# Kernel tuning notes

Hardware: AMD Instinct MI355X
Metric: run time of the kernel (lower is better)

## Reference

```python
import jax, jax.numpy as jnp
import numpy as np

LN_EPS = 1e-12


def _layernorm(x, gamma, beta):
    mu = jnp.mean(x, axis=-1, keepdims=True)
    var = jnp.var(x, axis=-1, keepdims=True)
    return gamma * (x - mu) / jnp.sqrt(var + LN_EPS) + beta


def setup_inputs() -> dict:
    key = jax.random.key(0)
    ks = jax.random.split(key, 8)
    B, N, C, H = 8, 8192, 512, 8
    FFN = 4 * C
    s_attn = 1.0 / np.sqrt(C)
    s_ffn1 = 1.0 / np.sqrt(C)
    s_ffn2 = 1.0 / np.sqrt(FFN)
    return {
        "x": jax.random.normal(ks[0], (B, N, C), jnp.float32),
        "wq": jax.random.normal(ks[1], (C, C), jnp.float32) * s_attn,
        "bq": jnp.zeros((C,), jnp.float32),
        "wk": jax.random.normal(ks[2], (C, C), jnp.float32) * s_attn,
        "bk": jnp.zeros((C,), jnp.float32),
        "wv": jax.random.normal(ks[3], (C, C), jnp.float32) * s_attn,
        "bv": jnp.zeros((C,), jnp.float32),
        "wo": jax.random.normal(ks[4], (C, C), jnp.float32) * s_attn,
        "bo": jnp.zeros((C,), jnp.float32),
        "gamma1": jnp.ones((C,), jnp.float32),
        "beta1": jnp.zeros((C,), jnp.float32),
        "w_fc1": jax.random.normal(ks[5], (C, FFN), jnp.float32) * s_ffn1,
        "b_fc1": jnp.zeros((FFN,), jnp.float32),
        "w_fc2": jax.random.normal(ks[6], (FFN, C), jnp.float32) * s_ffn2,
        "b_fc2": jnp.zeros((C,), jnp.float32),
        "gamma2": jnp.ones((C,), jnp.float32),
        "beta2": jnp.zeros((C,), jnp.float32),
        "window_size": 64,
        "n_head": 8,
    }


def reference(x, wq, bq, wk, bk, wv, bv, wo, bo, gamma1, beta1,
              w_fc1, b_fc1, w_fc2, b_fc2, gamma2, beta2,
              window_size, n_head):
    B, N, C = x.shape
    ws = window_size
    H = n_head
    dh = C // H

    # window partition: [B, N, C] -> [B*N/ws, ws, C]
    xw = x.reshape(B * N // ws, ws, C)
    shortcut = xw

    # windowed multi-head self-attention
    q = (xw @ wq + bq).reshape(-1, ws, H, dh)
    k = (xw @ wk + bk).reshape(-1, ws, H, dh)
    v = (xw @ wv + bv).reshape(-1, ws, H, dh)
    scale = 1.0 / jnp.sqrt(jnp.asarray(dh, xw.dtype))
    attn = jnp.einsum('wqhd,wkhd->whqk', q, k) * scale  # [nw, H, ws, ws]
    attn = jax.nn.softmax(attn, axis=-1)
    out = jnp.einsum('whqk,wkhd->wqhd', attn, v).reshape(-1, ws, C)
    out = out @ wo + bo

    # residual + LN1
    h = _layernorm(out + shortcut, gamma1, beta1)

    # MLP (fc1 -> GELU -> fc2), residual + LN2
    ff = jax.nn.gelu(h @ w_fc1 + b_fc1, approximate=False) @ w_fc2 + b_fc2
    h = _layernorm(ff + h, gamma2, beta2)

    # window reverse: -> [B, N, C]
    return h.reshape(B, N, C)
```

## Files before the change

kernel.cpp:

```cpp
#include <hip/hip_runtime.h>

typedef __attribute__((ext_vector_type(8))) short bf16x8;
typedef __attribute__((ext_vector_type(4))) float f32x4;

__device__ __forceinline__ short f2b(float f) {
  unsigned u = __builtin_bit_cast(unsigned, f);
  unsigned r = (u + 0x7FFFu + ((u >> 16) & 1u)) >> 16;
  return (short)r;
}
__device__ __forceinline__ float b2f(short s) {
  unsigned u = ((unsigned)(unsigned short)s) << 16;
  return __builtin_bit_cast(float, u);
}

__device__ __forceinline__ void gload16(const void* g, void* l) {
  __builtin_amdgcn_global_load_lds(
      (const __attribute__((address_space(1))) void*)g,
      (__attribute__((address_space(3))) void*)l, 16, 0, 0);
}

__device__ __forceinline__ float gelu_f(float v) {
  float u = v * (0.7978845608f + 0.0356774081f * v * v);
  float a = fabsf(u);
  float e = __expf(-2.f * a);
  float t = (1.f - e) * __builtin_amdgcn_rcpf(1.f + e);
  t = (u < 0.f) ? -t : t;
  return 0.5f * v * (1.f + t);
}

__global__ void cvt_bf16_vec(const float* __restrict__ src, short* __restrict__ dst, long n) {
  long i = ((long)blockIdx.x * 256 + threadIdx.x) * 8;
  if (i >= n) return;
  f32x4 a = *(const f32x4*)(src + i);
  f32x4 b = *(const f32x4*)(src + i + 4);
  bf16x8 o;
#pragma unroll
  for (int j = 0; j < 4; j++) o[j] = f2b(a[j]);
#pragma unroll
  for (int j = 0; j < 4; j++) o[j + 4] = f2b(b[j]);
  *(bf16x8*)(dst + i) = o;
}

__global__ void transpose_cvt_t(const float* __restrict__ src, short* __restrict__ dst,
                                int K, int N) {
  __shared__ float tile[32][33];
  const int n0 = blockIdx.x * 32, k0 = blockIdx.y * 32;
  const int j = threadIdx.x & 31, i0 = threadIdx.x >> 5;
#pragma unroll
  for (int r = 0; r < 4; r++) {
    int i = i0 + r * 8;
    tile[i][j] = src[(long)(k0 + i) * N + n0 + j];
  }
  __syncthreads();
#pragma unroll
  for (int r = 0; r < 4; r++) {
    int i = i0 + r * 8;
    dst[(long)(n0 + i) * K + k0 + j] = f2b(tile[j][i]);
  }
}

__global__ void pack_bias3(const float* __restrict__ b0, const float* __restrict__ b1,
                           const float* __restrict__ b2, float* __restrict__ out) {
  int t = blockIdx.x * 256 + threadIdx.x;
  if (t >= 1536) return;
  out[t] = (t < 512) ? b0[t] : ((t < 1024) ? b1[t - 512] : b2[t - 1024]);
}

template <int EPI>
__global__ __launch_bounds__(256, 3) void gemm_bt(
    const short* __restrict__ A, const short* __restrict__ Bt,
    const float* __restrict__ bias, const float* __restrict__ resF,
    const short* __restrict__ resB, void* __restrict__ Cout, int K, int ldc, int gxN) {
  __shared__ short lds[3 * 8192];
  const int t = threadIdx.x;
  const int w = t >> 6, lane = t & 63;
  const int lr = lane & 15, lg = lane >> 4;

  const int nwg = gridDim.x;
  const int orig = blockIdx.x;
  const int q = nwg >> 3, r = nwg & 7, xcd = orig & 7, idx = orig >> 3;
  const int swz = (xcd < r ? xcd * (q + 1) : r * (q + 1) + (xcd - r) * q) + idx;
  const long m0 = (long)(swz / gxN) * 128;
  const int n0 = (swz % gxN) * 128;

  const int wm = (w >> 1) * 64, wn = (w & 1) * 64;

  f32x4 acc[4][4];
#pragma unroll
  for (int i = 0; i < 4; i++)
#pragma unroll
    for (int j = 0; j < 4; j++) acc[i][j] = f32x4{0.f, 0.f, 0.f, 0.f};

  const int srow = t >> 2;
  const int schunk = (t & 3) ^ ((t >> 3) & 3);
  const short* Ag = A + (m0 + srow) * (long)K + schunk * 8;
  const short* Bg = Bt + ((long)n0 + srow) * K + schunk * 8;
  const long half = (long)64 * K;

#define STAGE(b, kt)                                   \
  {                                                    \
    short* d = lds + (b) * 8192 + t * 8;               \
    gload16(Ag + (long)(kt) * 32, d);                  \
    gload16(Ag + half + (long)(kt) * 32, d + 2048);    \
    gload16(Bg + (long)(kt) * 32, d + 4096);           \
    gload16(Bg + half + (long)(kt) * 32, d + 6144);    \
  }

  const int xsw = (lg ^ ((lr >> 1) & 3)) * 8;
  const int aoff = (wm + lr) * 32 + xsw;
  const int boff = 4096 + (wn + lr) * 32 + xsw;

#define TILE_WAIT(WN)                                        \
  asm volatile("s_waitcnt vmcnt(" #WN ")" ::: "memory");     \
  __builtin_amdgcn_sched_barrier(0);                         \
  __builtin_amdgcn_s_barrier();                              \
  __builtin_amdgcn_sched_barrier(0);

#define BODY(CB)                                                               \
  {                                                                            \
    const short* Lb = lds + (CB) * 8192;                                       \
    bf16x8 a[4], b[4];                                                         \
    _Pragma("unroll") for (int mi = 0; mi < 4; mi++)                           \
        a[mi] = *(const bf16x8*)(Lb + aoff + mi * 512);                        \
    _Pragma("unroll") for (int nj = 0; nj < 4; nj++)                           \
        b[nj] = *(const bf16x8*)(Lb + boff + nj * 512);                        \
    __builtin_amdgcn_s_setprio(1);                                             \
    _Pragma("unroll") for (int mi = 0; mi < 4; mi++)                           \
        _Pragma("unroll") for (int nj = 0; nj < 4; nj++) acc[mi][nj] =         \
            __builtin_amdgcn_mfma_f32_16x16x32_bf16(a[mi], b[nj], acc[mi][nj], \
                                                    0, 0, 0);                  \
    __builtin_amdgcn_s_setprio(0);                                             \
  }

  const int NKT = K >> 5;
  STAGE(0, 0)
  STAGE(1, 1)

  int cb = 0, sb = 2;
  for (int kt = 0; kt < NKT - 1; ++kt) {
    TILE_WAIT(4)
    if (kt + 2 < NKT) STAGE(sb, kt + 2)
    BODY(cb)
    cb = (cb == 2) ? 0 : cb + 1;
    sb = (sb == 2) ? 0 : sb + 1;
  }
  TILE_WAIT(0)
  BODY(cb)
#undef STAGE
#undef TILE_WAIT
#undef BODY

  float bv[4];
#pragma unroll
  for (int nj = 0; nj < 4; nj++) bv[nj] = bias[n0 + wn + nj * 16 + lr];

#pragma unroll
  for (int mi = 0; mi < 4; mi++)
#pragma unroll
    for (int i = 0; i < 4; i++) {
      const long row = m0 + wm + mi * 16 + lg * 4 + i;
      const long rb = row * ldc + n0 + wn + lr;
      if (EPI == 0) {
        short* p = (short*)Cout + rb;
#pragma unroll
        for (int nj = 0; nj < 4; nj++) p[nj * 16] = f2b(acc[mi][nj][i] + bv[nj]);
      } else if (EPI == 1) {
        short* p = (short*)Cout + rb;
#pragma unroll
        for (int nj = 0; nj < 4; nj++) p[nj * 16] = f2b(gelu_f(acc[mi][nj][i] + bv[nj]));
      } else if (EPI == 2) {
        short* p = (short*)Cout + rb;
        const float* rp = resF + rb;
#pragma unroll
        for (int nj = 0; nj < 4; nj++) p[nj * 16] = f2b(acc[mi][nj][i] + bv[nj] + rp[nj * 16]);
      } else {
        float* p = (float*)Cout + rb;
        const short* rp = resB + rb;
#pragma unroll
        for (int nj = 0; nj < 4; nj++)
          p[nj * 16] = acc[mi][nj][i] + bv[nj] + b2f(rp[nj * 16]);
      }
    }
}

#define DSR(d, a, OFF) \
  asm volatile("ds_read_b128 %0, %1 offset:" OFF : "=v"(d) : "v"(a))
#define SB __builtin_amdgcn_sched_barrier(0)

template <int EPI>
__global__ __launch_bounds__(512, 1) void gemm256(
    const short* __restrict__ A, const short* __restrict__ Bt,
    const float* __restrict__ bias, const float* __restrict__ resF,
    const short* __restrict__ resB, void* __restrict__ Cout, int K, int ldc, int gxN) {
  extern __shared__ short lds[];
  const int t = threadIdx.x;
  const int lane = t & 63, w = t >> 6;
  const int lr = lane & 15, lg = lane >> 4;
  const int wm = w >> 2, wn = w & 3;

  const int nwg = gridDim.x, orig = blockIdx.x;
  const int q8 = nwg >> 3, r8 = nwg & 7, xcd = orig & 7, idx = orig >> 3;
  const int swz = (xcd < r8 ? xcd * (q8 + 1) : r8 * (q8 + 1) + (xcd - r8) * q8) + idx;
  const long m0 = (long)(swz / gxN) * 256;
  const int n0 = (swz % gxN) * 256;

  f32x4 acc[8][4];
#pragma unroll
  for (int i = 0; i < 8; i++)
#pragma unroll
    for (int j = 0; j < 4; j++) acc[i][j] = f32x4{0.f, 0.f, 0.f, 0.f};

  const int srow = t >> 3;
  const int sch = (t & 7) ^ (srow & 7);
  const short* sA = A + (m0 + srow) * (long)K + sch * 8;
  const short* sB = Bt + ((long)n0 + srow) * K + sch * 8;
  const long r64 = (long)64 * K;

#define STG_A(tt, h)                                                     \
  {                                                                      \
    short* d_ = lds + ((tt) & 1) * 16384 + (h) * 8192 + t * 8;           \
    const short* s_ = sA + (h) * 2 * r64 + (long)(tt) * 64;              \
    gload16(s_, d_);                                                     \
    gload16(s_ + r64, d_ + 4096);                                        \
  }
#define STG_B(tt, h)                                                     \
  {                                                                      \
    short* d_ = lds + 32768 + ((tt) & 1) * 16384 + (h) * 8192 + t * 8;   \
    const short* s_ = sB + (h) * 2 * r64 + (long)(tt) * 64;              \
    gload16(s_, d_);                                                     \
    gload16(s_ + r64, d_ + 4096);                                        \
  }

  const unsigned ldsB = (unsigned)(uintptr_t)lds;
  const unsigned xb0 = (unsigned)((lg ^ (lr & 7)) * 16);
  const unsigned xb1 = (unsigned)(((4 + lg) ^ (lr & 7)) * 16);
  const unsigned aRowB = (unsigned)((wm * 128 + lr) * 128);
  const unsigned bRowB = 65536u + (unsigned)((wn * 64 + lr) * 128);

#define BAR                                  \
  {                                          \
    SB;                                      \
    __builtin_amdgcn_s_barrier();            \
    SB;                                      \
  }
#define LGKM0 asm volatile("s_waitcnt lgkmcnt(0)")

  const int NT = K >> 6;
  STG_A(0, 0) STG_A(0, 1) STG_B(0, 0) STG_B(0, 1) STG_B(1, 0) STG_B(1, 1)
  asm volatile("s_waitcnt vmcnt(4)" ::: "memory");
  BAR

#define MFMA8(AC, A0, A1)                                                      \
  {                                                                            \
    __builtin_amdgcn_s_setprio(1);                                             \
    acc[AC][0] = __builtin_amdgcn_mfma_f32_16x16x32_bf16(A0, b00, acc[AC][0], 0, 0, 0); \
    acc[AC][0] = __builtin_amdgcn_mfma_f32_16x16x32_bf16(A1, b01, acc[AC][0], 0, 0, 0); \
    acc[AC][1] = __builtin_amdgcn_mfma_f32_16x16x32_bf16(A0, b10, acc[AC][1], 0, 0, 0); \
    acc[AC][1] = __builtin_amdgcn_mfma_f32_16x16x32_bf16(A1, b11, acc[AC][1], 0, 0, 0); \
    acc[AC][2] = __builtin_amdgcn_mfma_f32_16x16x32_bf16(A0, b20, acc[AC][2], 0, 0, 0); \
    acc[AC][2] = __builtin_amdgcn_mfma_f32_16x16x32_bf16(A1, b21, acc[AC][2], 0, 0, 0); \
    acc[AC][3] = __builtin_amdgcn_mfma_f32_16x16x32_bf16(A0, b30, acc[AC][3], 0, 0, 0); \
    acc[AC][3] = __builtin_amdgcn_mfma_f32_16x16x32_bf16(A1, b31, acc[AC][3], 0, 0, 0); \
    __builtin_amdgcn_s_setprio(0);                                             \
  }

  for (int tt = 0; tt < NT; ++tt) {
    const unsigned dAb = (unsigned)((tt & 1) * 32768);
    const unsigned aA0 = ldsB + aRowB + xb0 + dAb;
    const unsigned aA1 = ldsB + aRowB + xb1 + dAb;
    const unsigned bA0 = ldsB + bRowB + xb0 + dAb;
    const unsigned bA1 = ldsB + bRowB + xb1 + dAb;
    bf16x8 b00, b01, b10, b11, b20, b21, b30, b31;

    {
      DSR(b00, bA0, "0");    DSR(b01, bA1, "0");
      DSR(b10, bA0, "2048"); DSR(b11, bA1, "2048");
      DSR(b20, bA0, "4096"); DSR(b21, bA1, "4096");
      DSR(b30, bA0, "6144"); DSR(b31, bA1, "6144");
      bf16x8 a00, a01, a10, a11;
      DSR(a00, aA0, "0");    DSR(a01, aA1, "0");
      DSR(a10, aA0, "2048"); DSR(a11, aA1, "2048");
      SB;
      if (tt + 1 < NT) STG_A(tt + 1, 0)
      BAR
      LGKM0; SB;
      MFMA8(0, a00, a01)
      MFMA8(1, a10, a11)
      BAR
    }
    {
      bf16x8 a00, a01, a10, a11;
      DSR(a00, aA0, "4096"); DSR(a01, aA1, "4096");
      DSR(a10, aA0, "6144"); DSR(a11, aA1, "6144");
      SB;
      if (tt + 1 < NT) STG_A(tt + 1, 1)
      BAR
      LGKM0; SB;
      MFMA8(2, a00, a01)
      MFMA8(3, a10, a11)
      BAR
    }
    {
      bf16x8 a00, a01, a10, a11;
      DSR(a00, aA0, "8192");  DSR(a01, aA1, "8192");
      DSR(a10, aA0, "10240"); DSR(a11, aA1, "10240");
      SB;
      if (tt + 2 < NT) STG_B(tt + 2, 0)
      BAR
      LGKM0; SB;
      MFMA8(4, a00, a01)
      MFMA8(5, a10, a11)
      BAR
    }
    {
      bf16x8 a00, a01, a10, a11;
      DSR(a00, aA0, "12288"); DSR(a01, aA1, "12288");
      DSR(a10, aA0, "14336"); DSR(a11, aA1, "14336");
      SB;
      if (tt + 2 < NT) STG_B(tt + 2, 1)
      BAR
      LGKM0; SB;
      MFMA8(6, a00, a01)
      MFMA8(7, a10, a11)
      if (tt + 2 < NT) {
        asm volatile("s_waitcnt vmcnt(4)" ::: "memory");
      } else if (tt + 1 < NT) {
        asm volatile("s_waitcnt vmcnt(0)" ::: "memory");
      }
      BAR
    }
  }
#undef MFMA8
#undef STG_A
#undef STG_B

  float bv[4];
#pragma unroll
  for (int nj = 0; nj < 4; nj++) bv[nj] = bias[n0 + wn * 64 + nj * 16 + lr];

#pragma unroll
  for (int a = 0; a < 8; a++)
#pragma unroll
    for (int i = 0; i < 4; i++) {
      const long row = m0 + wm * 128 + a * 16 + lg * 4 + i;
      const long rb = row * ldc + n0 + wn * 64 + lr;
      if (EPI == 0) {
        short* p = (short*)Cout + rb;
#pragma unroll
        for (int nj = 0; nj < 4; nj++) p[nj * 16] = f2b(acc[a][nj][i] + bv[nj]);
      } else if (EPI == 1) {
        short* p = (short*)Cout + rb;
#pragma unroll
        for (int nj = 0; nj < 4; nj++) p[nj * 16] = f2b(gelu_f(acc[a][nj][i] + bv[nj]));
      } else if (EPI == 2) {
        short* p = (short*)Cout + rb;
        const float* rp = resF + rb;
#pragma unroll
        for (int nj = 0; nj < 4; nj++)
          p[nj * 16] = f2b(acc[a][nj][i] + bv[nj] + rp[nj * 16]);
      } else {
        float* p = (float*)Cout + rb;
        const short* rp = resB + rb;
#pragma unroll
        for (int nj = 0; nj < 4; nj++)
          p[nj * 16] = acc[a][nj][i] + bv[nj] + b2f(rp[nj * 16]);
      }
    }
}
#undef DSR
#undef SB
#undef BAR
#undef LGKM0

__global__ __launch_bounds__(256, 2) void attn_win(const short* __restrict__ QKV,
                                                   short* __restrict__ AO) {
  __shared__ short Vs[64 * 72];
  __shared__ short Ps[64 * 72];
  const int t = threadIdx.x, w = t >> 6, lane = t & 63;
  const int lr = lane & 15, lg = lane >> 4;
  const long base = (long)blockIdx.x * 64 * 1536;
  const long obase = (long)blockIdx.x * 64 * 512;

  for (int h = 0; h < 8; h++) {
    const int co = h * 64;
#pragma unroll
    for (int it = 0; it < 2; it++) {
      int c = t + it * 256;
      int j = c >> 3, d0 = (c & 7) * 8;
      *(bf16x8*)(Vs + j * 72 + d0) =
          *(const bf16x8*)(QKV + base + (long)j * 1536 + 1024 + co + d0);
    }
    __syncthreads();

    bf16x8 qf[2], kf[4][2];
#pragma unroll
    for (int kb = 0; kb < 2; kb++)
      qf[kb] = *(const bf16x8*)(QKV + base + (long)(w * 16 + lr) * 1536 + co + kb * 32 + lg * 8);
#pragma unroll
    for (int nj = 0; nj < 4; nj++)
#pragma unroll
      for (int kb = 0; kb < 2; kb++)
        kf[nj][kb] = *(const bf16x8*)(QKV + base + (long)(nj * 16 + lr) * 1536 + 512 + co +
                                      kb * 32 + lg * 8);

    f32x4 s[4];
#pragma unroll
    for (int nj = 0; nj < 4; nj++) {
      s[nj] = f32x4{0.f, 0.f, 0.f, 0.f};
      s[nj] = __builtin_amdgcn_mfma_f32_16x16x32_bf16(qf[0], kf[nj][0], s[nj], 0, 0, 0);
      s[nj] = __builtin_amdgcn_mfma_f32_16x16x32_bf16(qf[1], kf[nj][1], s[nj], 0, 0, 0);
      s[nj] = s[nj] * 0.125f;
    }

#pragma unroll
    for (int i = 0; i < 4; i++) {
      float mx = fmaxf(fmaxf(s[0][i], s[1][i]), fmaxf(s[2][i], s[3][i]));
#pragma unroll
      for (int off = 1; off < 16; off <<= 1) mx = fmaxf(mx, __shfl_xor(mx, off, 64));
      float sum = 0.f;
#pragma unroll
      for (int nj = 0; nj < 4; nj++) {
        float p = __expf(s[nj][i] - mx);
        s[nj][i] = p;
        sum += p;
      }
#pragma unroll
      for (int off = 1; off < 16; off <<= 1) sum += __shfl_xor(sum, off, 64);
      float inv = 1.f / sum;
#pragma unroll
      for (int nj = 0; nj < 4; nj++) s[nj][i] *= inv;
    }

#pragma unroll
    for (int nj = 0; nj < 4; nj++)
#pragma unroll
      for (int i = 0; i < 4; i++)
        Ps[(w * 16 + lg * 4 + i) * 72 + nj * 16 + lr] = f2b(s[nj][i]);

    bf16x8 pa[2];
#pragma unroll
    for (int kb = 0; kb < 2; kb++)
      pa[kb] = *(const bf16x8*)(Ps + (w * 16 + lr) * 72 + kb * 32 + lg * 8);

    f32x4 o[4];
#pragma unroll
    for (int nb = 0; nb < 4; nb++) o[nb] = f32x4{0.f, 0.f, 0.f, 0.f};
#pragma unroll
    for (int kb = 0; kb < 2; kb++)
#pragma unroll
      for (int nb = 0; nb < 4; nb++) {
        bf16x8 vb;
#pragma unroll
        for (int jj = 0; jj < 8; jj++)
          vb[jj] = Vs[(kb * 32 + lg * 8 + jj) * 72 + nb * 16 + lr];
        o[nb] = __builtin_amdgcn_mfma_f32_16x16x32_bf16(pa[kb], vb, o[nb], 0, 0, 0);
      }

#pragma unroll
    for (int nb = 0; nb < 4; nb++)
#pragma unroll
      for (int i = 0; i < 4; i++)
        AO[obase + (long)(w * 16 + lg * 4 + i) * 512 + co + nb * 16 + lr] = f2b(o[nb][i]);
    __syncthreads();
  }
}

template <int INB, int OUTB>
__global__ __launch_bounds__(256, 4) void ln_rows(const float* __restrict__ Yf,
                                                  const short* __restrict__ Yb,
                                                  const float* __restrict__ gamma,
                                                  const float* __restrict__ beta,
                                                  short* __restrict__ Hb,
                                                  float* __restrict__ Of) {
  const int w = threadIdx.x >> 6, lane = threadIdx.x & 63;
  const long row = (long)blockIdx.x * 4 + w;
  float v[8];
  if (INB) {
    bf16x8 x = *(const bf16x8*)(Yb + row * 512 + lane * 8);
#pragma unroll
    for (int j = 0; j < 8; j++) v[j] = b2f(x[j]);
  } else {
    f32x4 a = *(const f32x4*)(Yf + row * 512 + lane * 8);
    f32x4 b = *(const f32x4*)(Yf + row * 512 + lane * 8 + 4);
#pragma unroll
    for (int j = 0; j < 4; j++) { v[j] = a[j]; v[j + 4] = b[j]; }
  }
  float s = 0.f, s2 = 0.f;
#pragma unroll
  for (int j = 0; j < 8; j++) { s += v[j]; s2 += v[j] * v[j]; }
#pragma unroll
  for (int off = 1; off < 64; off <<= 1) {
    s += __shfl_xor(s, off, 64);
    s2 += __shfl_xor(s2, off, 64);
  }
  float mu = s * (1.f / 512.f);
  float var = s2 * (1.f / 512.f) - mu * mu;
  float rstd = rsqrtf(fmaxf(var, 0.f) + 1e-12f);
  const int c0 = lane * 8;
  f32x4 ga = *(const f32x4*)(gamma + c0), gb = *(const f32x4*)(gamma + c0 + 4);
  f32x4 ba = *(const f32x4*)(beta + c0), bb = *(const f32x4*)(beta + c0 + 4);
  if (OUTB) {
    bf16x8 o;
#pragma unroll
    for (int j = 0; j < 4; j++) o[j] = f2b(ga[j] * ((v[j] - mu) * rstd) + ba[j]);
#pragma unroll
    for (int j = 0; j < 4; j++) o[j + 4] = f2b(gb[j] * ((v[j + 4] - mu) * rstd) + bb[j]);
    *(bf16x8*)(Hb + row * 512 + c0) = o;
  } else {
    f32x4 o0, o1;
#pragma unroll
    for (int j = 0; j < 4; j++) o0[j] = ga[j] * ((v[j] - mu) * rstd) + ba[j];
#pragma unroll
    for (int j = 0; j < 4; j++) o1[j] = gb[j] * ((v[j + 4] - mu) * rstd) + bb[j];
    *(f32x4*)(Of + row * 512 + c0) = o0;
    *(f32x4*)(Of + row * 512 + c0 + 4) = o1;
  }
}

extern "C" void kernel_launch(void* const* d_in, const int* in_sizes, int n_in,
                              void* d_out, int out_size, void* d_ws, size_t ws_size,
                              hipStream_t stream) {
  (void)in_sizes; (void)n_in; (void)out_size;
  const float* x = (const float*)d_in[0];
  const float* wq = (const float*)d_in[1];
  const float* bq = (const float*)d_in[2];
  const float* wk = (const float*)d_in[3];
  const float* bk = (const float*)d_in[4];
  const float* wv = (const float*)d_in[5];
  const float* bv = (const float*)d_in[6];
  const float* wo = (const float*)d_in[7];
  const float* bo = (const float*)d_in[8];
  const float* g1 = (const float*)d_in[9];
  const float* be1 = (const float*)d_in[10];
  const float* wfc1 = (const float*)d_in[11];
  const float* bfc1 = (const float*)d_in[12];
  const float* wfc2 = (const float*)d_in[13];
  const float* bfc2 = (const float*)d_in[14];
  const float* g2 = (const float*)d_in[15];
  const float* be2 = (const float*)d_in[16];

  const long T = 65536;
  char* ws = (char*)d_ws;

  short* WQKVT = (short*)(ws);
  short* WOT = WQKVT + 1536 * 512;
  short* WFC1T = WOT + 512 * 512;
  short* WFC2T = WFC1T + 2048 * 512;
  float* BQKV = (float*)(WFC2T + 512 * 2048);
  size_t woff = ((size_t)((char*)(BQKV + 1536) - ws) + 255) & ~(size_t)255;

  size_t avail = (ws_size > woff) ? (ws_size - woff) : 0;
  long Tc = T;
  while (Tc > 256 && (size_t)Tc * 7168 > avail) Tc >>= 1;
  const long nch = T / Tc;

  char* R0 = ws + woff;
  char* R1 = R0 + (size_t)Tc * 4096;
  char* R2 = R1 + (size_t)Tc * 2048;

  short* QKV = (short*)R0;
  short* Y1b = (short*)R0;
  short* FF1 = (short*)R0;
  short* XB = (short*)R1;
  short* AO = (short*)R1;
  float* Y2 = (float*)R1;
  short* H = (short*)R2;

  transpose_cvt_t<<<dim3(16, 16), 256, 0, stream>>>(wq, WQKVT, 512, 512);
  transpose_cvt_t<<<dim3(16, 16), 256, 0, stream>>>(wk, WQKVT + 512 * 512, 512, 512);
  transpose_cvt_t<<<dim3(16, 16), 256, 0, stream>>>(wv, WQKVT + 1024 * 512, 512, 512);
  transpose_cvt_t<<<dim3(16, 16), 256, 0, stream>>>(wo, WOT, 512, 512);
  transpose_cvt_t<<<dim3(64, 16), 256, 0, stream>>>(wfc1, WFC1T, 512, 2048);
  transpose_cvt_t<<<dim3(16, 64), 256, 0, stream>>>(wfc2, WFC2T, 2048, 512);
  pack_bias3<<<6, 256, 0, stream>>>(bq, bk, bv, BQKV);

  const size_t LDSB = 131072;
  for (long c = 0; c < nch; c++) {
    const long t0 = c * Tc;
    const int mb = (int)(Tc / 256);
    const int mb2 = (int)(Tc / 128);
    cvt_bf16_vec<<<(int)(Tc / 4), 256, 0, stream>>>(x + t0 * 512, XB, Tc * 512);
    gemm256<0><<<mb * 6, 512, LDSB, stream>>>(XB, WQKVT, BQKV, nullptr, nullptr,
                                              (void*)QKV, 512, 1536, 6);
    attn_win<<<(int)(Tc / 64), 256, 0, stream>>>(QKV, AO);
    gemm256<2><<<mb * 2, 512, LDSB, stream>>>(AO, WOT, bo, x + t0 * 512, nullptr,
                                              (void*)Y1b, 512, 512, 2);
    ln_rows<1, 1><<<(int)(Tc / 4), 256, 0, stream>>>(nullptr, Y1b, g1, be1, H, nullptr);
    gemm_bt<1><<<mb2 * 16, 256, 0, stream>>>(H, WFC1T, bfc1, nullptr, nullptr,
                                             (void*)FF1, 512, 2048, 16);
    gemm256<3><<<mb * 2, 512, LDSB, stream>>>(FF1, WFC2T, bfc2, nullptr, H, (void*)Y2,
                                              2048, 512, 2);
    ln_rows<0, 0><<<(int)(Tc / 4), 256, 0, stream>>>(Y2, nullptr, g2, be2, nullptr,
                                                     (float*)d_out + t0 * 512);
  }
}
```

Baseline: 761.6 us.

## Merge weight packing, use bf16 residuals and Y2, transpose V in LDS

Replaces the six weight transpose launches with a single pack_all kernel. The out-projection residual now reads bf16 XB instead of fp32 x, and the fc2 output is stored as bf16 and fed to LN2 as bf16 input. This halves residual and intermediate traffic at some precision cost. The attention kernel also transposes V into a separate LDS buffer so the PV MFMA operand is one 128-bit load instead of eight scalar reads, at the cost of extra LDS and barriers.

Result: faster. 731.3 us (-4.0%).

```diff
diff --git a/kernel.cpp b/kernel.cpp
--- a/kernel.cpp
+++ b/kernel.cpp
@@ -41,10 +41,24 @@
   *(bf16x8*)(dst + i) = o;
 }
 
-__global__ void transpose_cvt_t(const float* __restrict__ src, short* __restrict__ dst,
-                                int K, int N) {
+__global__ void pack_all(const float* __restrict__ wq, const float* __restrict__ wk,
+                         const float* __restrict__ wv, const float* __restrict__ wo,
+                         const float* __restrict__ wfc1, const float* __restrict__ wfc2,
+                         short* __restrict__ WQKVT, short* __restrict__ WOT,
+                         short* __restrict__ WFC1T, short* __restrict__ WFC2T) {
   __shared__ float tile[32][33];
-  const int n0 = blockIdx.x * 32, k0 = blockIdx.y * 32;
+  const int b = blockIdx.x;
+  const float* src;
+  short* dst;
+  int K, N, tb;
+  if (b < 256)       { src = wq;   dst = WQKVT;             K = 512;  N = 512;  tb = b; }
+  else if (b < 512)  { src = wk;   dst = WQKVT + 512 * 512; K = 512;  N = 512;  tb = b - 256; }
+  else if (b < 768)  { src = wv;   dst = WQKVT + 1024 * 512; K = 512; N = 512;  tb = b - 512; }
+  else if (b < 1024) { src = wo;   dst = WOT;               K = 512;  N = 512;  tb = b - 768; }
+  else if (b < 2048) { src = wfc1; dst = WFC1T;             K = 512;  N = 2048; tb = b - 1024; }
+  else               { src = wfc2; dst = WFC2T;             K = 2048; N = 512;  tb = b - 2048; }
+  const int ntx = N >> 5;
+  const int n0 = (tb % ntx) * 32, k0 = (tb / ntx) * 32;
   const int j = threadIdx.x & 31, i0 = threadIdx.x >> 5;
 #pragma unroll
   for (int r = 0; r < 4; r++) {
@@ -69,8 +83,7 @@
 template <int EPI>
 __global__ __launch_bounds__(256, 3) void gemm_bt(
     const short* __restrict__ A, const short* __restrict__ Bt,
-    const float* __restrict__ bias, const float* __restrict__ resF,
-    const short* __restrict__ resB, void* __restrict__ Cout, int K, int ldc, int gxN) {
+    const float* __restrict__ bias, void* __restrict__ Cout, int K, int ldc, int gxN) {
   __shared__ short lds[3 * 8192];
   const int t = threadIdx.x;
   const int w = t >> 6, lane = t & 63;
@@ -160,26 +173,9 @@
     for (int i = 0; i < 4; i++) {
       const long row = m0 + wm + mi * 16 + lg * 4 + i;
       const long rb = row * ldc + n0 + wn + lr;
-      if (EPI == 0) {
-        short* p = (short*)Cout + rb;
-#pragma unroll
-        for (int nj = 0; nj < 4; nj++) p[nj * 16] = f2b(acc[mi][nj][i] + bv[nj]);
-      } else if (EPI == 1) {
-        short* p = (short*)Cout + rb;
-#pragma unroll
-        for (int nj = 0; nj < 4; nj++) p[nj * 16] = f2b(gelu_f(acc[mi][nj][i] + bv[nj]));
-      } else if (EPI == 2) {
-        short* p = (short*)Cout + rb;
-        const float* rp = resF + rb;
-#pragma unroll
-        for (int nj = 0; nj < 4; nj++) p[nj * 16] = f2b(acc[mi][nj][i] + bv[nj] + rp[nj * 16]);
-      } else {
-        float* p = (float*)Cout + rb;
-        const short* rp = resB + rb;
-#pragma unroll
-        for (int nj = 0; nj < 4; nj++)
-          p[nj * 16] = acc[mi][nj][i] + bv[nj] + b2f(rp[nj * 16]);
-      }
+      short* p = (short*)Cout + rb;
+#pragma unroll
+      for (int nj = 0; nj < 4; nj++) p[nj * 16] = f2b(gelu_f(acc[mi][nj][i] + bv[nj]));
     }
 }
 
@@ -190,8 +186,8 @@
 template <int EPI>
 __global__ __launch_bounds__(512, 1) void gemm256(
     const short* __restrict__ A, const short* __restrict__ Bt,
-    const float* __restrict__ bias, const float* __restrict__ resF,
-    const short* __restrict__ resB, void* __restrict__ Cout, int K, int ldc, int gxN) {
+    const float* __restrict__ bias, const short* __restrict__ resB,
+    void* __restrict__ Cout, int K, int ldc, int gxN) {
   extern __shared__ short lds[];
   const int t = threadIdx.x;
   const int lane = t & 63, w = t >> 6;
@@ -344,26 +340,15 @@
     for (int i = 0; i < 4; i++) {
       const long row = m0 + wm * 128 + a * 16 + lg * 4 + i;
       const long rb = row * ldc + n0 + wn * 64 + lr;
+      short* p = (short*)Cout + rb;
       if (EPI == 0) {
-        short* p = (short*)Cout + rb;
 #pragma unroll
         for (int nj = 0; nj < 4; nj++) p[nj * 16] = f2b(acc[a][nj][i] + bv[nj]);
-      } else if (EPI == 1) {
-        short* p = (short*)Cout + rb;
-#pragma unroll
-        for (int nj = 0; nj < 4; nj++) p[nj * 16] = f2b(gelu_f(acc[a][nj][i] + bv[nj]));
-      } else if (EPI == 2) {
-        short* p = (short*)Cout + rb;
-        const float* rp = resF + rb;
+      } else {
+        const short* rp = resB + rb;
 #pragma unroll
         for (int nj = 0; nj < 4; nj++)
-          p[nj * 16] = f2b(acc[a][nj][i] + bv[nj] + rp[nj * 16]);
-      } else {
-        float* p = (float*)Cout + rb;
-        const short* rp = resB + rb;
-#pragma unroll
-        for (int nj = 0; nj < 4; nj++)
-          p[nj * 16] = acc[a][nj][i] + bv[nj] + b2f(rp[nj * 16]);
+          p[nj * 16] = f2b(acc[a][nj][i] + bv[nj] + b2f(rp[nj * 16]));
       }
     }
 }
@@ -375,6 +360,7 @@
 __global__ __launch_bounds__(256, 2) void attn_win(const short* __restrict__ QKV,
                                                    short* __restrict__ AO) {
   __shared__ short Vs[64 * 72];
+  __shared__ short Vt[64 * 72];
   __shared__ short Ps[64 * 72];
   const int t = threadIdx.x, w = t >> 6, lane = t & 63;
   const int lr = lane & 15, lg = lane >> 4;
@@ -390,8 +376,6 @@
       *(bf16x8*)(Vs + j * 72 + d0) =
           *(const bf16x8*)(QKV + base + (long)j * 1536 + 1024 + co + d0);
     }
-    __syncthreads();
-
     bf16x8 qf[2], kf[4][2];
 #pragma unroll
     for (int kb = 0; kb < 2; kb++)
@@ -402,6 +386,17 @@
       for (int kb = 0; kb < 2; kb++)
         kf[nj][kb] = *(const bf16x8*)(QKV + base + (long)(nj * 16 + lr) * 1536 + 512 + co +
                                       kb * 32 + lg * 8);
+    __syncthreads();
+
+#pragma unroll
+    for (int it2 = 0; it2 < 2; it2++) {
+      int d = t & 63;
+      int j0 = ((t >> 6) + it2 * 4) * 8;
+      bf16x8 tmp;
+#pragma unroll
+      for (int jj = 0; jj < 8; jj++) tmp[jj] = Vs[(j0 + jj) * 72 + d];
+      *(bf16x8*)(Vt + d * 72 + j0) = tmp;
+    }
 
     f32x4 s[4];
 #pragma unroll
@@ -437,6 +432,8 @@
       for (int i = 0; i < 4; i++)
         Ps[(w * 16 + lg * 4 + i) * 72 + nj * 16 + lr] = f2b(s[nj][i]);
 
+    __syncthreads();
+
     bf16x8 pa[2];
 #pragma unroll
     for (int kb = 0; kb < 2; kb++)
@@ -449,10 +446,7 @@
     for (int kb = 0; kb < 2; kb++)
 #pragma unroll
       for (int nb = 0; nb < 4; nb++) {
-        bf16x8 vb;
-#pragma unroll
-        for (int jj = 0; jj < 8; jj++)
-          vb[jj] = Vs[(kb * 32 + lg * 8 + jj) * 72 + nb * 16 + lr];
+        bf16x8 vb = *(const bf16x8*)(Vt + (nb * 16 + lr) * 72 + kb * 32 + lg * 8);
         o[nb] = __builtin_amdgcn_mfma_f32_16x16x32_bf16(pa[kb], vb, o[nb], 0, 0, 0);
       }
 
@@ -556,22 +550,18 @@
 
   char* R0 = ws + woff;
   char* R1 = R0 + (size_t)Tc * 4096;
-  char* R2 = R1 + (size_t)Tc * 2048;
+  char* R1b = R1 + (size_t)Tc * 1024;
+  char* R2 = R1b + (size_t)Tc * 1024;
 
   short* QKV = (short*)R0;
   short* Y1b = (short*)R0;
   short* FF1 = (short*)R0;
   short* XB = (short*)R1;
-  short* AO = (short*)R1;
-  float* Y2 = (float*)R1;
+  short* AO = (short*)R1b;
+  short* Y2b = (short*)R1b;
   short* H = (short*)R2;
 
-  transpose_cvt_t<<<dim3(16, 16), 256, 0, stream>>>(wq, WQKVT, 512, 512);
-  transpose_cvt_t<<<dim3(16, 16), 256, 0, stream>>>(wk, WQKVT + 512 * 512, 512, 512);
-  transpose_cvt_t<<<dim3(16, 16), 256, 0, stream>>>(wv, WQKVT + 1024 * 512, 512, 512);
-  transpose_cvt_t<<<dim3(16, 16), 256, 0, stream>>>(wo, WOT, 512, 512);
-  transpose_cvt_t<<<dim3(64, 16), 256, 0, stream>>>(wfc1, WFC1T, 512, 2048);
-  transpose_cvt_t<<<dim3(16, 64), 256, 0, stream>>>(wfc2, WFC2T, 2048, 512);
+  pack_all<<<3072, 256, 0, stream>>>(wq, wk, wv, wo, wfc1, wfc2, WQKVT, WOT, WFC1T, WFC2T);
   pack_bias3<<<6, 256, 0, stream>>>(bq, bk, bv, BQKV);
 
   const size_t LDSB = 131072;
@@ -580,17 +570,16 @@
     const int mb = (int)(Tc / 256);
     const int mb2 = (int)(Tc / 128);
     cvt_bf16_vec<<<(int)(Tc / 4), 256, 0, stream>>>(x + t0 * 512, XB, Tc * 512);
-    gemm256<0><<<mb * 6, 512, LDSB, stream>>>(XB, WQKVT, BQKV, nullptr, nullptr,
+    gemm256<0><<<mb * 6, 512, LDSB, stream>>>(XB, WQKVT, BQKV, nullptr,
                                               (void*)QKV, 512, 1536, 6);
     attn_win<<<(int)(Tc / 64), 256, 0, stream>>>(QKV, AO);
-    gemm256<2><<<mb * 2, 512, LDSB, stream>>>(AO, WOT, bo, x + t0 * 512, nullptr,
+    gemm256<2><<<mb * 2, 512, LDSB, stream>>>(AO, WOT, bo, XB,
                                               (void*)Y1b, 512, 512, 2);
     ln_rows<1, 1><<<(int)(Tc / 4), 256, 0, stream>>>(nullptr, Y1b, g1, be1, H, nullptr);
-    gemm_bt<1><<<mb2 * 16, 256, 0, stream>>>(H, WFC1T, bfc1, nullptr, nullptr,
-                                             (void*)FF1, 512, 2048, 16);
-    gemm256<3><<<mb * 2, 512, LDSB, stream>>>(FF1, WFC2T, bfc2, nullptr, H, (void*)Y2,
-                                              2048, 512, 2);
-    ln_rows<0, 0><<<(int)(Tc / 4), 256, 0, stream>>>(Y2, nullptr, g2, be2, nullptr,
+    gemm_bt<1><<<mb2 * 16, 256, 0, stream>>>(H, WFC1T, bfc1, (void*)FF1, 512, 2048, 16);
+    gemm256<2><<<mb * 2, 512, LDSB, stream>>>(FF1, WFC2T, bfc2, H,
+                                              (void*)Y2b, 2048, 512, 2);
+    ln_rows<1, 0><<<(int)(Tc / 4), 256, 0, stream>>>(nullptr, Y2b, g2, be2, nullptr,
                                                      (float*)d_out + t0 * 512);
   }
 }
```
